# Optimization experiments

Hardware: AMD Instinct MI355X
Metric: run time of the kernel (lower is better)

The kernel has to match this reference:

```python
import jax, jax.numpy as jnp
import numpy as np

COMMITMENT_COST = 0.25
NUM_EMBEDDINGS = 8192
EMBEDDING_DIM = 64


def setup_inputs() -> dict:
    key = jax.random.key(0)
    k1, k2 = jax.random.split(key)
    z_e = jax.random.normal(k1, (32, 1024, EMBEDDING_DIM), dtype=jnp.float32)
    # nn.Embedding init: uniform(-1/num_embeddings, 1/num_embeddings)
    lim = 1.0 / NUM_EMBEDDINGS
    weight = jax.random.uniform(k2, (NUM_EMBEDDINGS, EMBEDDING_DIM), dtype=jnp.float32,
                                minval=-lim, maxval=lim)
    return {"z_e": z_e, "weight": weight}


def reference(z_e, weight):
    B = z_e.shape[0]
    D = weight.shape[1]
    z_flat = z_e.reshape(-1, D)  # [T, D], T = B*N
    # squared euclidean distances: ||z||^2 + ||e||^2 - 2 z e^T  -> [T, K]
    distances = (jnp.sum(z_flat ** 2, axis=1, keepdims=True)
                 + jnp.sum(weight ** 2, axis=1)
                 - 2.0 * jnp.matmul(z_flat, weight.T))
    encoding_indices = jnp.argmin(distances, axis=1)  # [T]
    # direct gather == one-hot @ weight (same math, no dense one-hot)
    z_q = weight[encoding_indices].reshape(z_e.shape)
    loss_1 = jnp.mean((jax.lax.stop_gradient(z_e) - z_q) ** 2)
    loss_2 = jnp.mean((z_e - jax.lax.stop_gradient(z_q)) ** 2)
    vq_loss = loss_1 + COMMITMENT_COST * loss_2
    # straight-through estimator
    z_q_st = z_e + jax.lax.stop_gradient(z_q - z_e)
    return (z_q_st, vq_loss)
```

## Files before the change

kernel.cpp:

```cpp
#include <hip/hip_runtime.h>

typedef float f32x16 __attribute__((ext_vector_type(16)));
typedef int v8i __attribute__((ext_vector_type(8)));

#define NUM_EMB 8192
#define DIM 64
#define NTOK 32768
#define TOKS_PER_BLOCK 32
#define TOK_BLOCKS 1024
#define CHUNKS_PER_WAVE 64

#define B_SCALE (-8192.0f)
#define SCORE_BIAS 128.0f

__device__ __forceinline__ unsigned umin2(unsigned a, unsigned b) { return a < b ? a : b; }

__global__ __launch_bounds__(256) void vq_prep(const float* __restrict__ weight,
                                               uint4* __restrict__ wsB,
                                               float* __restrict__ loss_out) {
  int m = blockIdx.x * 256 + threadIdx.x;
  if (m == 0)
    __hip_atomic_store(loss_out, 0.0f, __ATOMIC_RELAXED, __HIP_MEMORY_SCOPE_AGENT);
  int lane = m & 63, h = (m >> 6) & 1, c = m >> 7;
  int n = c * 32 + (lane & 31);
  int kb = (lane >> 5) * 8;
  const float* p = weight + n * DIM;
  unsigned r[4];
#pragma unroll
  for (int q = 0; q < 2; ++q) {
    const float* pk = p + (2 * h + q) * 16 + kb;
    int lo = __builtin_amdgcn_cvt_pk_fp8_f32(B_SCALE * pk[0], B_SCALE * pk[1], 0, false);
    lo     = __builtin_amdgcn_cvt_pk_fp8_f32(B_SCALE * pk[2], B_SCALE * pk[3], lo, true);
    int hi = __builtin_amdgcn_cvt_pk_fp8_f32(B_SCALE * pk[4], B_SCALE * pk[5], 0, false);
    hi     = __builtin_amdgcn_cvt_pk_fp8_f32(B_SCALE * pk[6], B_SCALE * pk[7], hi, true);
    r[q * 2] = (unsigned)lo; r[q * 2 + 1] = (unsigned)hi;
  }
  wsB[m] = make_uint4(r[0], r[1], r[2], r[3]);
}

__global__ __launch_bounds__(256, 4) void vq_main(const float* __restrict__ z_e,
                                                  const float* __restrict__ weight,
                                                  const uint4* __restrict__ wsB,
                                                  float* __restrict__ out,
                                                  float* __restrict__ loss_out) {
  __shared__ unsigned char lds_a[TOKS_PER_BLOCK * 72];
  __shared__ unsigned lds_part[4][TOKS_PER_BLOCK];
  __shared__ unsigned lds_tok[TOKS_PER_BLOCK];
  __shared__ float wsum[4];

  const int tid  = threadIdx.x;
  const int lane = tid & 63;
  const int wave = tid >> 6;
  const int half = lane >> 5;
  const int ln31 = lane & 31;
  const int tbase = blockIdx.x * TOKS_PER_BLOCK;

  {
    int token = tid >> 3, g = tid & 7;
    const float* p = z_e + (size_t)(tbase + token) * DIM + g * 8;
    float4 x0 = *reinterpret_cast<const float4*>(p);
    float4 x1 = *reinterpret_cast<const float4*>(p + 4);
    int lo = __builtin_amdgcn_cvt_pk_fp8_f32(x0.x, x0.y, 0, false);
    lo     = __builtin_amdgcn_cvt_pk_fp8_f32(x0.z, x0.w, lo, true);
    int hi = __builtin_amdgcn_cvt_pk_fp8_f32(x1.x, x1.y, 0, false);
    hi     = __builtin_amdgcn_cvt_pk_fp8_f32(x1.z, x1.w, hi, true);
    *reinterpret_cast<uint2*>(&lds_a[token * 72 + g * 8]) = make_uint2((unsigned)lo, (unsigned)hi);
  }
  __syncthreads();

  v8i a8;
  {
    union { uint2 d2[4]; v8i v; } au;
#pragma unroll
    for (int f = 0; f < 4; ++f)
      au.d2[f] = *reinterpret_cast<const uint2*>(&lds_a[ln31 * 72 + f * 16 + half * 8]);
    a8 = au.v;
  }

  f32x16 bias;
#pragma unroll
  for (int i = 0; i < 16; ++i) bias[i] = SCORE_BIAS;

  unsigned run[16];
#pragma unroll
  for (int i = 0; i < 16; ++i) run[i] = 0xFFFFFFFFu;

  const int c0 = wave * CHUNKS_PER_WAVE;
  unsigned idx = (unsigned)(c0 * 32 + ln31);

  uint4 bA = wsB[(c0 * 2 + 0) * 64 + lane];
  uint4 bB = wsB[(c0 * 2 + 1) * 64 + lane];

  for (int c = 0; c < CHUNKS_PER_WAVE; ++c) {
    int cn = c0 + c + 1;
    uint4 nA = wsB[(cn * 2 + 0) * 64 + lane];
    uint4 nB = wsB[(cn * 2 + 1) * 64 + lane];

    union { uint4 q[2]; v8i v; } bu;
    bu.q[0] = bA; bu.q[1] = bB;

    f32x16 acc = __builtin_amdgcn_mfma_scale_f32_32x32x64_f8f6f4(
        a8, bu.v, bias, 0 , 0 , 0, 0x7F, 0, 0x7F);

#pragma unroll
    for (int i = 0; i < 16; ++i)
      run[i] = umin2(run[i], (__float_as_uint(acc[i]) & 0xFFFFE000u) | idx);
    idx += 32;
    bA = nA; bB = nB;
  }

#pragma unroll
  for (int i = 0; i < 16; ++i) {
    unsigned v = run[i];
    v = umin2(v, (unsigned)__builtin_amdgcn_ds_swizzle((int)v, 0x041F));
    v = umin2(v, (unsigned)__builtin_amdgcn_ds_swizzle((int)v, 0x081F));
    v = umin2(v, (unsigned)__builtin_amdgcn_ds_swizzle((int)v, 0x101F));
    v = umin2(v, (unsigned)__builtin_amdgcn_ds_swizzle((int)v, 0x201F));
    v = umin2(v, (unsigned)__builtin_amdgcn_ds_swizzle((int)v, 0x401F));
    run[i] = v;
  }

  if (ln31 == 0) {
#pragma unroll
    for (int reg = 0; reg < 16; ++reg) {
      int row = (reg & 3) + 8 * (reg >> 2) + 4 * half;
      lds_part[wave][row] = run[reg];
    }
  }
  __syncthreads();

  if (tid < TOKS_PER_BLOCK) {
    unsigned k = umin2(umin2(lds_part[0][tid], lds_part[1][tid]),
                       umin2(lds_part[2][tid], lds_part[3][tid]));
    lds_tok[tid] = k & 0x1FFFu;
  }
  __syncthreads();

  const float4* z4 = reinterpret_cast<const float4*>(z_e);
  const float4* w4 = reinterpret_cast<const float4*>(weight);
  float4* o4 = reinterpret_cast<float4*>(out);
  float lsum = 0.0f;
#pragma unroll
  for (int r = 0; r < 2; ++r) {
    int g = r * 256 + tid;
    int t = g >> 4, q = g & 15;
    float4 z = z4[(size_t)tbase * 16 + g];
    float4 w = w4[(size_t)lds_tok[t] * 16 + q];
    float4 o;
    o.x = z.x + (w.x - z.x); o.y = z.y + (w.y - z.y);
    o.z = z.z + (w.z - z.z); o.w = z.w + (w.w - z.w);
    o4[(size_t)tbase * 16 + g] = o;
    float dx = z.x - w.x, dy = z.y - w.y, dz = z.z - w.z, dw = z.w - w.w;
    lsum += dx * dx + dy * dy + dz * dz + dw * dw;
  }
#pragma unroll
  for (int s = 32; s >= 1; s >>= 1) lsum += __shfl_xor(lsum, s, 64);
  if (lane == 0) wsum[wave] = lsum;
  __syncthreads();
  if (tid == 0)
    atomicAdd(loss_out, (wsum[0] + wsum[1] + wsum[2] + wsum[3]) * (1.25f / 2097152.0f));
}

extern "C" void kernel_launch(void* const* d_in, const int* in_sizes, int n_in,
                              void* d_out, int out_size, void* d_ws, size_t ws_size,
                              hipStream_t stream) {
  const float* z_e    = (const float*)d_in[0];
  const float* weight = (const float*)d_in[1];
  float* out  = (float*)d_out;
  float* loss = out + (out_size - 1);
  uint4* wsB = (uint4*)d_ws;

  vq_prep<<<128, 256, 0, stream>>>(weight, wsB, loss);
  vq_main<<<TOK_BLOCKS, 256, 0, stream>>>(z_e, weight, wsB, out, loss);
}
```

Measured before the change: 94.37 us.

## Share codebook chunks across token tiles via double-buffered LDS staging

Each block now handles 128 tokens with 16 waves instead of 32 tokens with 4 waves. Waves are arranged as a 4x4 grid of token tiles by codebook groups. Each step loads an 8 KB codebook superchunk into LDS with global_load_lds, double-buffered, and four token-tile waves read the same chunk. This cuts redundant global/L2 reads of the FP8 codebook by sharing them across token tiles. The cost is a block-wide barrier every iteration and only one large block per CU, which may expose load latency and barrier stalls.

```diff
diff --git a/kernel.cpp b/kernel.cpp
--- a/kernel.cpp
+++ b/kernel.cpp
@@ -6,9 +6,10 @@
 #define NUM_EMB 8192
 #define DIM 64
 #define NTOK 32768
-#define TOKS_PER_BLOCK 32
-#define TOK_BLOCKS 1024
-#define CHUNKS_PER_WAVE 64
+#define TOKS_PER_BLOCK 128
+#define TOK_BLOCKS 256
+#define SUPER 64
+#define SUPER_BYTES 8192
 
 #define B_SCALE (-8192.0f)
 #define SCORE_BIAS 128.0f
@@ -38,33 +39,44 @@
   wsB[m] = make_uint4(r[0], r[1], r[2], r[3]);
 }
 
-__global__ __launch_bounds__(256, 4) void vq_main(const float* __restrict__ z_e,
-                                                  const float* __restrict__ weight,
-                                                  const uint4* __restrict__ wsB,
-                                                  float* __restrict__ out,
-                                                  float* __restrict__ loss_out) {
+__global__ __launch_bounds__(1024) void vq_main(const float* __restrict__ z_e,
+                                                const float* __restrict__ weight,
+                                                const uint4* __restrict__ wsB,
+                                                float* __restrict__ out,
+                                                float* __restrict__ loss_out) {
   __shared__ unsigned char lds_a[TOKS_PER_BLOCK * 72];
+  __shared__ unsigned char bbuf[2][SUPER_BYTES];
   __shared__ unsigned lds_part[4][TOKS_PER_BLOCK];
   __shared__ unsigned lds_tok[TOKS_PER_BLOCK];
-  __shared__ float wsum[4];
+  __shared__ float wsum[16];
 
   const int tid  = threadIdx.x;
   const int lane = tid & 63;
-  const int wave = tid >> 6;
+  const int wv   = tid >> 6;
+  const int row4 = wv & 3;
+  const int g    = wv >> 2;
   const int half = lane >> 5;
   const int ln31 = lane & 31;
   const int tbase = blockIdx.x * TOKS_PER_BLOCK;
 
+  const unsigned char* wsb_bytes = reinterpret_cast<const unsigned char*>(wsB);
+
   {
-    int token = tid >> 3, g = tid & 7;
-    const float* p = z_e + (size_t)(tbase + token) * DIM + g * 8;
+    int token = tid >> 3, q8 = tid & 7;
+    const float* p = z_e + (size_t)(tbase + token) * DIM + q8 * 8;
     float4 x0 = *reinterpret_cast<const float4*>(p);
     float4 x1 = *reinterpret_cast<const float4*>(p + 4);
     int lo = __builtin_amdgcn_cvt_pk_fp8_f32(x0.x, x0.y, 0, false);
     lo     = __builtin_amdgcn_cvt_pk_fp8_f32(x0.z, x0.w, lo, true);
     int hi = __builtin_amdgcn_cvt_pk_fp8_f32(x1.x, x1.y, 0, false);
     hi     = __builtin_amdgcn_cvt_pk_fp8_f32(x1.z, x1.w, hi, true);
-    *reinterpret_cast<uint2*>(&lds_a[token * 72 + g * 8]) = make_uint2((unsigned)lo, (unsigned)hi);
+    *reinterpret_cast<uint2*>(&lds_a[token * 72 + q8 * 8]) = make_uint2((unsigned)lo, (unsigned)hi);
+  }
+  if (wv < 8) {
+    const unsigned char* src = wsb_bytes + 0 * SUPER_BYTES + wv * 1024 + lane * 16;
+    __builtin_amdgcn_global_load_lds(
+        (const __attribute__((address_space(1))) void*)src,
+        (__attribute__((address_space(3))) void*)&bbuf[0][wv * 1024], 16, 0, 0);
   }
   __syncthreads();
 
@@ -73,7 +85,7 @@
     union { uint2 d2[4]; v8i v; } au;
 #pragma unroll
     for (int f = 0; f < 4; ++f)
-      au.d2[f] = *reinterpret_cast<const uint2*>(&lds_a[ln31 * 72 + f * 16 + half * 8]);
+      au.d2[f] = *reinterpret_cast<const uint2*>(&lds_a[(row4 * 32 + ln31) * 72 + f * 16 + half * 8]);
     a8 = au.v;
   }
 
@@ -85,19 +97,20 @@
 #pragma unroll
   for (int i = 0; i < 16; ++i) run[i] = 0xFFFFFFFFu;
 
-  const int c0 = wave * CHUNKS_PER_WAVE;
-  unsigned idx = (unsigned)(c0 * 32 + ln31);
+  unsigned idx = (unsigned)(g * 32 + ln31);
 
-  uint4 bA = wsB[(c0 * 2 + 0) * 64 + lane];
-  uint4 bB = wsB[(c0 * 2 + 1) * 64 + lane];
-
-  for (int c = 0; c < CHUNKS_PER_WAVE; ++c) {
-    int cn = c0 + c + 1;
-    uint4 nA = wsB[(cn * 2 + 0) * 64 + lane];
-    uint4 nB = wsB[(cn * 2 + 1) * 64 + lane];
+  for (int t = 0; t < SUPER; ++t) {
+    int p = t & 1;
+    if (wv < 8) {
+      const unsigned char* src = wsb_bytes + (size_t)(t + 1) * SUPER_BYTES + wv * 1024 + lane * 16;
+      __builtin_amdgcn_global_load_lds(
+          (const __attribute__((address_space(1))) void*)src,
+          (__attribute__((address_space(3))) void*)&bbuf[1 - p][wv * 1024], 16, 0, 0);
+    }
 
     union { uint4 q[2]; v8i v; } bu;
-    bu.q[0] = bA; bu.q[1] = bB;
+    bu.q[0] = *reinterpret_cast<const uint4*>(&bbuf[p][g * 2048 + (lane << 4)]);
+    bu.q[1] = *reinterpret_cast<const uint4*>(&bbuf[p][g * 2048 + 1024 + (lane << 4)]);
 
     f32x16 acc = __builtin_amdgcn_mfma_scale_f32_32x32x64_f8f6f4(
         a8, bu.v, bias, 0 , 0 , 0, 0x7F, 0, 0x7F);
@@ -105,8 +118,9 @@
 #pragma unroll
     for (int i = 0; i < 16; ++i)
       run[i] = umin2(run[i], (__float_as_uint(acc[i]) & 0xFFFFE000u) | idx);
-    idx += 32;
-    bA = nA; bB = nB;
+    idx += 128;
+
+    __syncthreads();
   }
 
 #pragma unroll
@@ -124,7 +138,7 @@
 #pragma unroll
     for (int reg = 0; reg < 16; ++reg) {
       int row = (reg & 3) + 8 * (reg >> 2) + 4 * half;
-      lds_part[wave][row] = run[reg];
+      lds_part[g][row4 * 32 + row] = run[reg];
     }
   }
   __syncthreads();
@@ -142,23 +156,27 @@
   float lsum = 0.0f;
 #pragma unroll
   for (int r = 0; r < 2; ++r) {
-    int g = r * 256 + tid;
-    int t = g >> 4, q = g & 15;
-    float4 z = z4[(size_t)tbase * 16 + g];
+    int gg = r * 1024 + tid;
+    int t = gg >> 4, q = gg & 15;
+    float4 z = z4[(size_t)tbase * 16 + gg];
     float4 w = w4[(size_t)lds_tok[t] * 16 + q];
     float4 o;
     o.x = z.x + (w.x - z.x); o.y = z.y + (w.y - z.y);
     o.z = z.z + (w.z - z.z); o.w = z.w + (w.w - z.w);
-    o4[(size_t)tbase * 16 + g] = o;
+    o4[(size_t)tbase * 16 + gg] = o;
     float dx = z.x - w.x, dy = z.y - w.y, dz = z.z - w.z, dw = z.w - w.w;
     lsum += dx * dx + dy * dy + dz * dz + dw * dw;
   }
 #pragma unroll
   for (int s = 32; s >= 1; s >>= 1) lsum += __shfl_xor(lsum, s, 64);
-  if (lane == 0) wsum[wave] = lsum;
+  if (lane == 0) wsum[wv] = lsum;
   __syncthreads();
-  if (tid == 0)
-    atomicAdd(loss_out, (wsum[0] + wsum[1] + wsum[2] + wsum[3]) * (1.25f / 2097152.0f));
+  if (tid == 0) {
+    float tot = 0.0f;
+#pragma unroll
+    for (int i = 0; i < 16; ++i) tot += wsum[i];
+    atomicAdd(loss_out, tot * (1.25f / 2097152.0f));
+  }
 }
 
 extern "C" void kernel_launch(void* const* d_in, const int* in_sizes, int n_in,
@@ -171,5 +189,5 @@
   uint4* wsB = (uint4*)d_ws;
 
   vq_prep<<<128, 256, 0, stream>>>(weight, wsB, loss);
-  vq_main<<<TOK_BLOCKS, 256, 0, stream>>>(z_e, weight, wsB, out, loss);
+  vq_main<<<TOK_BLOCKS, 1024, 0, stream>>>(z_e, weight, wsB, out, loss);
 }
```

Result: slower. 102.7 us (+8.9%).
